# Optimization experiments

Hardware: AMD Instinct MI355X
Metric: run time of the kernel (lower is better)

The kernel has to match this reference:

```python
import jax, jax.numpy as jnp
import numpy as np

B, T, D_IN, D_OUT = 4, 2048, 1024, 1024


def setup_inputs() -> dict:
    key = jax.random.key(0)
    k1, k2, k3, k4 = jax.random.split(key, 4)
    s = 0.02  # keep activations in a sane range
    x = jax.random.normal(k1, (B, T, D_IN), dtype=jnp.float32)
    Wq = jax.random.normal(k2, (D_IN, D_OUT), dtype=jnp.float32) * s
    Wk = jax.random.normal(k3, (D_IN, D_OUT), dtype=jnp.float32) * s
    Wv = jax.random.normal(k4, (D_IN, D_OUT), dtype=jnp.float32) * s
    return {"x": x, "Wq": Wq, "Wk": Wk, "Wv": Wv}


def reference(x, Wq, Wk, Wv):
    # Linear projections (torch Linear: y = x @ W^T, here W stored as [d_in, d_out])
    q = jnp.einsum('btd,de->bte', x, Wq)
    k = jnp.einsum('btd,de,->bte', x, Wk, jnp.float32(1.0)) if False else jnp.einsum('btd,de->bte', x, Wk)
    v = jnp.einsum('btd,de->bte', x, Wv)
    # Full [B, T, T] score matrix (faithful to the hand-rolled implementation)
    scores = jnp.einsum('bqe,bke->bqk', q, k)
    T_ = x.shape[1]
    causal = jnp.triu(jnp.ones((T_, T_), dtype=bool), k=1)  # True above diagonal
    scores = jnp.where(causal[None, :, :], -jnp.inf, scores)
    scale = 1.0 / jnp.sqrt(jnp.asarray(k.shape[-1], dtype=scores.dtype))
    attn = jax.nn.softmax(scores * scale, axis=-1)
    # dropout p=0.0 -> identity
    return jnp.einsum('bqk,bke->bqe', attn, v)
```

## Files before the change

### kernel.cpp

```cpp
#include <hip/hip_runtime.h>
#include <hip/hip_bf16.h>
#include <cstdint>

typedef __attribute__((ext_vector_type(8))) short short8;
typedef __attribute__((ext_vector_type(4))) float floatx4;
typedef unsigned short ushort;

__device__ __forceinline__ float bf2f(ushort u) {
  unsigned int x = ((unsigned int)u) << 16;
  return __builtin_bit_cast(float, x);
}
__device__ __forceinline__ ushort f2bf(float f) {
  unsigned int x = __builtin_bit_cast(unsigned int, f);
  x += 0x7fffu + ((x >> 16) & 1u);
  return (ushort)(x >> 16);
}

__device__ __forceinline__ void gload_lds16(const void* g, void* l) {
  __builtin_amdgcn_global_load_lds(
      (const __attribute__((address_space(1))) void*)g,
      (__attribute__((address_space(3))) void*)l, 16, 0, 0);
}


__global__ __launch_bounds__(256) void cvtx_kernel(const float* __restrict__ x,
                                                   ushort* __restrict__ xb) {
  int i = blockIdx.x * 256 + threadIdx.x;
  const float4* xf = (const float4*)x;
  float4 a = xf[i * 2], b = xf[i * 2 + 1];
  short8 o;
  o[0] = (short)f2bf(a.x); o[1] = (short)f2bf(a.y);
  o[2] = (short)f2bf(a.z); o[3] = (short)f2bf(a.w);
  o[4] = (short)f2bf(b.x); o[5] = (short)f2bf(b.y);
  o[6] = (short)f2bf(b.z); o[7] = (short)f2bf(b.w);
  ((short8*)xb)[i] = o;
}

__global__ __launch_bounds__(256) void wt_kernel(const float* __restrict__ Wq,
                                                 const float* __restrict__ Wk,
                                                 const float* __restrict__ Wv,
                                                 ushort* __restrict__ Wt) {
  int z = blockIdx.z;
  const float* W = z == 0 ? Wq : (z == 1 ? Wk : Wv);
  ushort* O = Wt + (size_t)z * 1024 * 1024;
  __shared__ float tile[64][65];
  int c0 = blockIdx.x * 64;
  int r0 = blockIdx.y * 64;
  int tid = threadIdx.x;
#pragma unroll
  for (int i = 0; i < 4; ++i) {
    int c = tid + i * 256; int rr = c >> 4, q = c & 15;
    float4 v = *(const float4*)&W[(size_t)(r0 + rr) * 1024 + c0 + q * 4];
    tile[rr][q * 4 + 0] = v.x; tile[rr][q * 4 + 1] = v.y;
    tile[rr][q * 4 + 2] = v.z; tile[rr][q * 4 + 3] = v.w;
  }
  __syncthreads();
#pragma unroll
  for (int i = 0; i < 2; ++i) {
    int c = tid + i * 256; int oc = c >> 3, q = c & 7;
    short8 o;
#pragma unroll
    for (int j = 0; j < 8; ++j) o[j] = (short)f2bf(tile[q * 8 + j][oc]);
    *(short8*)&O[(size_t)(c0 + oc) * 1024 + r0 + q * 8] = o;
  }
}

__global__ __launch_bounds__(256) void vt_kernel(const ushort* __restrict__ V,
                                                 ushort* __restrict__ Vt) {
  int b = blockIdx.z;
  const ushort* Vb = V + (size_t)b * 2048 * 1024;
  ushort* Vtb = Vt + (size_t)b * 1024 * 2048;
  __shared__ ushort tile[64][72];
  int t0 = blockIdx.x * 64;
  int e0 = blockIdx.y * 64;
  int tid = threadIdx.x;
#pragma unroll
  for (int i = 0; i < 2; ++i) {
    int c = tid + i * 256; int rr = c >> 3, q = c & 7;
    short8 s = *(const short8*)&Vb[(size_t)(t0 + rr) * 1024 + e0 + q * 8];
#pragma unroll
    for (int j = 0; j < 8; ++j) tile[rr][q * 8 + j] = (ushort)s[j];
  }
  __syncthreads();
#pragma unroll
  for (int i = 0; i < 2; ++i) {
    int c = tid + i * 256; int er = c >> 3, q = c & 7;
    short8 o;
#pragma unroll
    for (int j = 0; j < 8; ++j) o[j] = (short)tile[q * 8 + j][er];
    *(short8*)&Vtb[(size_t)(e0 + er) * 2048 + t0 + q * 8] = o;
  }
}


__global__ __launch_bounds__(512, 2) void qkv8_kernel(const ushort* __restrict__ A,
                                                      const ushort* __restrict__ Bm,
                                                      ushort* __restrict__ QKV) {
  __shared__ __align__(16) ushort lds[2][2][2][8192];

  const int tid = threadIdx.x;
  const int lane = tid & 63;
  const int wave = tid >> 6;
  const int wm = wave >> 2;
  const int wn = wave & 3;
  const int r15 = lane & 15;
  const int kg = lane >> 4;

  const int nwgx = 32, nwgy = 12;
  int orig = blockIdx.y * nwgx + blockIdx.x;
  int swz = (orig & 7) * ((nwgx * nwgy) >> 3) + (orig >> 3);
  int by = swz % nwgy;
  int bx = swz / nwgy;
  const int m0 = bx * 256;
  const int n0 = by * 256;

  const ushort* Ag = A + (size_t)m0 * 1024;
  const ushort* Bg = Bm + (size_t)n0 * 1024;

  const int NKT = 16;

  floatx4 acc[8][4] = {};

  auto stage = [&](int sidx) {
    int kt = sidx >> 2, hh = sidx & 3;
    int mat = hh & 1, kh = hh >> 1;
    ushort* dst = &lds[kt & 1][mat][kh][0];
    const ushort* src = mat ? Bg : Ag;
    int kbase = kt * 64 + kh * 32;
#pragma unroll
    for (int i = 0; i < 2; ++i) {
      int t = tid + i * 512;
      int d = t * 16;
      int L = d ^ (((d >> 7) & 3) << 4);
      int row = L >> 6;
      int colE = (L & 63) >> 1;
      gload_lds16(src + (size_t)row * 1024 + kbase + colE, dst + t * 8);
    }
  };

  auto ldA = [&](int buf, int ks, int m) -> short8 {
    int row = wm * 128 + m * 16 + r15;
    int L = row * 64 + kg * 16;
    int P = L ^ (((row >> 1) & 3) << 4);
    return *(const short8*)((const char*)&lds[buf][0][ks][0] + P);
  };
  auto ldB = [&](int buf, int ks, int n) -> short8 {
    int row = wn * 64 + n * 16 + r15;
    int L = row * 64 + kg * 16;
    int P = L ^ (((row >> 1) & 3) << 4);
    return *(const short8*)((const char*)&lds[buf][1][ks][0] + P);
  };

  for (int s = 0; s < 6; ++s) stage(s);
  asm volatile("s_waitcnt vmcnt(8)" ::: "memory");
  __builtin_amdgcn_s_barrier();

  short8 bfrag[4];
  int sidx = 6;
  for (int kt = 0; kt < NKT; ++kt) {
    int cur = kt & 1;
#pragma unroll
    for (int q = 0; q < 4; ++q) {
      const int ks = q >> 1;
      const int msub = (q & 1) * 4;
      short8 afrag[4];
      if ((q & 1) == 0) {
#pragma unroll
        for (int n = 0; n < 4; ++n) bfrag[n] = ldB(cur, ks, n);
      }
#pragma unroll
      for (int m = 0; m < 4; ++m) afrag[m] = ldA(cur, ks, msub + m);
      if (sidx < NKT * 4) stage(sidx);
      ++sidx;
      if (q & 1) asm volatile("s_waitcnt vmcnt(4)" ::: "memory");
      __builtin_amdgcn_s_barrier();
      asm volatile("s_waitcnt lgkmcnt(0)" ::: "memory");
      __builtin_amdgcn_sched_barrier(0);
      __builtin_amdgcn_s_setprio(1);
#pragma unroll
      for (int m = 0; m < 4; ++m)
#pragma unroll
        for (int n = 0; n < 4; ++n)
          acc[msub + m][n] =
              __builtin_amdgcn_mfma_f32_16x16x32_bf16(afrag[m], bfrag[n], acc[msub + m][n], 0, 0, 0);
      __builtin_amdgcn_s_setprio(0);
      __builtin_amdgcn_s_barrier();
    }
  }

  ushort* Cz = QKV + (size_t)(n0 >> 10) * 8192 * 1024;
  const int cb = n0 & 1023;
  const int rq = kg * 4;
#pragma unroll
  for (int m = 0; m < 8; ++m) {
#pragma unroll
    for (int n = 0; n < 4; ++n) {
      int gc = cb + wn * 64 + n * 16 + r15;
#pragma unroll
      for (int r = 0; r < 4; ++r) {
        int gr = m0 + wm * 128 + m * 16 + rq + r;
        Cz[(size_t)gr * 1024 + gc] = f2bf(acc[m][n][r]);
      }
    }
  }
}


template <bool OUT_BF16>
__device__ __forceinline__ void gemm_tn_core(const ushort* __restrict__ A,
                                             const ushort* __restrict__ B,
                                             void* __restrict__ C,
                                             int lda, int ldb, int ldc,
                                             int m0, int n0, int kTiles) {
  __shared__ __align__(16) ushort Asm[2][128 * 32];
  __shared__ __align__(16) ushort Bsm[2][128 * 32];
  const int tid = threadIdx.x;
  const int lane = tid & 63;
  const int wave = tid >> 6;
  const int wrow = (wave >> 1) * 64;
  const int wcol = (wave & 1) * 64;
  const int r15 = lane & 15;
  const int kg = (lane >> 4) * 8;

  floatx4 acc[4][4] = {};

  const ushort* Ag = A + (size_t)m0 * lda;
  const ushort* Bg = B + (size_t)n0 * ldb;

  auto stage = [&](int buf, int kt) {
    int k0 = kt * 32;
#pragma unroll
    for (int i = 0; i < 2; ++i) {
      int c = tid + i * 256;
      gload_lds16(Ag + (size_t)(c >> 2) * lda + k0 + (c & 3) * 8, &Asm[buf][c * 8]);
    }
#pragma unroll
    for (int i = 0; i < 2; ++i) {
      int c = tid + i * 256;
      gload_lds16(Bg + (size_t)(c >> 2) * ldb + k0 + (c & 3) * 8, &Bsm[buf][c * 8]);
    }
  };

  stage(0, 0);
  for (int kt = 0; kt < kTiles; ++kt) {
    int cur = kt & 1;
    __syncthreads();
    if (kt + 1 < kTiles) stage(cur ^ 1, kt + 1);
    const ushort* As = Asm[cur];
    const ushort* Bs = Bsm[cur];
    short8 af[4], bfr[4];
#pragma unroll
    for (int m = 0; m < 4; ++m)
      af[m] = *(const short8*)&As[(wrow + m * 16 + r15) * 32 + kg];
#pragma unroll
    for (int n = 0; n < 4; ++n)
      bfr[n] = *(const short8*)&Bs[(wcol + n * 16 + r15) * 32 + kg];
#pragma unroll
    for (int m = 0; m < 4; ++m)
#pragma unroll
      for (int n = 0; n < 4; ++n)
        acc[m][n] = __builtin_amdgcn_mfma_f32_16x16x32_bf16(af[m], bfr[n], acc[m][n], 0, 0, 0);
  }

  const int rq = (lane >> 4) * 4;
#pragma unroll
  for (int m = 0; m < 4; ++m) {
#pragma unroll
    for (int n = 0; n < 4; ++n) {
      int gc = n0 + wcol + n * 16 + r15;
#pragma unroll
      for (int r = 0; r < 4; ++r) {
        int gr = m0 + wrow + m * 16 + rq + r;
        if (OUT_BF16)
          ((ushort*)C)[(size_t)gr * ldc + gc] = f2bf(acc[m][n][r]);
        else
          ((float*)C)[(size_t)gr * ldc + gc] = acc[m][n][r];
      }
    }
  }
}

__global__ __launch_bounds__(256) void s_kernel(const ushort* __restrict__ Q,
                                                const ushort* __restrict__ K,
                                                ushort* __restrict__ S) {
  int t = blockIdx.x;
  int qb = (int)((sqrtf(8.f * (float)t + 1.f) - 1.f) * 0.5f);
  while ((qb + 1) * (qb + 2) / 2 <= t) ++qb;
  while (qb * (qb + 1) / 2 > t) --qb;
  int kb = t - qb * (qb + 1) / 2;
  size_t b = blockIdx.y;
  gemm_tn_core<true>(Q + b * 2048 * 1024, K + b * 2048 * 1024, S + b * 2048 * 2048,
                     1024, 1024, 2048, qb * 128, kb * 128, 32);
}

__global__ __launch_bounds__(256) void pv_kernel(const ushort* __restrict__ P,
                                                 const ushort* __restrict__ Vt,
                                                 float* __restrict__ O) {
  int qb = blockIdx.x;
  size_t b = blockIdx.z;
  gemm_tn_core<false>(P + b * 2048 * 2048, Vt + b * 1024 * 2048, O + b * 2048 * 1024,
                      2048, 2048, 1024, qb * 128, blockIdx.y * 128, (qb + 1) * 4);
}

__global__ __launch_bounds__(256) void softmax_kernel(ushort* __restrict__ S) {
  const int r = blockIdx.x;
  const int b = blockIdx.y;
  ushort* row = S + ((size_t)b * 2048 + r) * 2048;
  const int len = r + 1;
  const int padEnd = ((r >> 7) + 1) << 7;
  const int tid = threadIdx.x;
  const int base = tid * 8;
  const float scale = 0.03125f;

  float v[8];
  float mymax = -1e30f;
  if (base < len) {
    short8 s = *(const short8*)(row + base);
#pragma unroll
    for (int j = 0; j < 8; ++j) {
      float f = (base + j < len) ? bf2f((ushort)s[j]) : -1e30f;
      v[j] = f;
      mymax = fmaxf(mymax, f);
    }
  } else {
#pragma unroll
    for (int j = 0; j < 8; ++j) v[j] = -1e30f;
  }

  __shared__ float redm[4], reds[4];
  const int wave = tid >> 6, lane = tid & 63;
#pragma unroll
  for (int off = 32; off > 0; off >>= 1) mymax = fmaxf(mymax, __shfl_xor(mymax, off, 64));
  if (lane == 0) redm[wave] = mymax;
  __syncthreads();
  float m = fmaxf(fmaxf(redm[0], redm[1]), fmaxf(redm[2], redm[3])) * scale;

  float p[8];
  float mysum = 0.f;
#pragma unroll
  for (int j = 0; j < 8; ++j) {
    float e = (base + j < len) ? __expf(v[j] * scale - m) : 0.f;
    p[j] = e;
    mysum += e;
  }
#pragma unroll
  for (int off = 32; off > 0; off >>= 1) mysum += __shfl_xor(mysum, off, 64);
  if (lane == 0) reds[wave] = mysum;
  __syncthreads();
  float inv = 1.f / (reds[0] + reds[1] + reds[2] + reds[3]);

  if (base < padEnd) {
    short8 o;
#pragma unroll
    for (int j = 0; j < 8; ++j) o[j] = (short)f2bf(p[j] * inv);
    *(short8*)(row + base) = o;
  }
}


extern "C" void kernel_launch(void* const* d_in, const int* in_sizes, int n_in,
                              void* d_out, int out_size, void* d_ws, size_t ws_size,
                              hipStream_t stream) {
  const float* x  = (const float*)d_in[0];
  const float* Wq = (const float*)d_in[1];
  const float* Wk = (const float*)d_in[2];
  const float* Wv = (const float*)d_in[3];
  float* out = (float*)d_out;

  ushort* Xb  = (ushort*)d_ws;
  ushort* Wt  = Xb + (size_t)8192 * 1024;
  ushort* QKV = Wt + (size_t)3 * 1024 * 1024;
  ushort* Vt  = QKV + (size_t)3 * 8192 * 1024;
  ushort* S   = Vt + (size_t)4 * 1024 * 2048;

  const ushort* Qp = QKV;
  const ushort* Kp = QKV + (size_t)8192 * 1024;
  const ushort* Vp = QKV + (size_t)2 * 8192 * 1024;

  hipLaunchKernelGGL(cvtx_kernel, dim3(4096), dim3(256), 0, stream, x, Xb);
  hipLaunchKernelGGL(wt_kernel, dim3(16, 16, 3), dim3(256), 0, stream, Wq, Wk, Wv, Wt);
  hipLaunchKernelGGL(qkv8_kernel, dim3(32, 12), dim3(512), 0, stream, Xb, Wt, QKV);
  hipLaunchKernelGGL(vt_kernel, dim3(32, 16, 4), dim3(256), 0, stream, Vp, Vt);
  hipLaunchKernelGGL(s_kernel, dim3(136, 4), dim3(256), 0, stream, Qp, Kp, S);
  hipLaunchKernelGGL(softmax_kernel, dim3(2048, 4), dim3(256), 0, stream, S);
  hipLaunchKernelGGL(pv_kernel, dim3(16, 8, 4), dim3(256), 0, stream, S, Vt, out);
}
```

Baseline: 188.7 us.

## Fuse V transpose into QKV GEMM epilogue and retile to 128x256 triple-buffered

```diff
diff --git a/kernel.cpp b/kernel.cpp
--- a/kernel.cpp
+++ b/kernel.cpp
@@ -3,6 +3,7 @@
 #include <cstdint>
 
 typedef __attribute__((ext_vector_type(8))) short short8;
+typedef __attribute__((ext_vector_type(4))) short short4v;
 typedef __attribute__((ext_vector_type(4))) float floatx4;
 typedef unsigned short ushort;
 
@@ -65,141 +66,147 @@
   }
 }
 
-__global__ __launch_bounds__(256) void vt_kernel(const ushort* __restrict__ V,
-                                                 ushort* __restrict__ Vt) {
-  int b = blockIdx.z;
-  const ushort* Vb = V + (size_t)b * 2048 * 1024;
-  ushort* Vtb = Vt + (size_t)b * 1024 * 2048;
-  __shared__ ushort tile[64][72];
-  int t0 = blockIdx.x * 64;
-  int e0 = blockIdx.y * 64;
-  int tid = threadIdx.x;
-#pragma unroll
-  for (int i = 0; i < 2; ++i) {
-    int c = tid + i * 256; int rr = c >> 3, q = c & 7;
-    short8 s = *(const short8*)&Vb[(size_t)(t0 + rr) * 1024 + e0 + q * 8];
-#pragma unroll
-    for (int j = 0; j < 8; ++j) tile[rr][q * 8 + j] = (ushort)s[j];
-  }
-  __syncthreads();
-#pragma unroll
-  for (int i = 0; i < 2; ++i) {
-    int c = tid + i * 256; int er = c >> 3, q = c & 7;
-    short8 o;
-#pragma unroll
-    for (int j = 0; j < 8; ++j) o[j] = (short)tile[q * 8 + j][er];
-    *(short8*)&Vtb[(size_t)(e0 + er) * 2048 + t0 + q * 8] = o;
-  }
-}
-
-
-__global__ __launch_bounds__(512, 2) void qkv8_kernel(const ushort* __restrict__ A,
+
+__global__ __launch_bounds__(256, 2) void qkv2_kernel(const ushort* __restrict__ A,
                                                       const ushort* __restrict__ Bm,
-                                                      ushort* __restrict__ QKV) {
-  __shared__ __align__(16) ushort lds[2][2][2][8192];
+                                                      ushort* __restrict__ Qo,
+                                                      ushort* __restrict__ Ko,
+                                                      ushort* __restrict__ Vt) {
+  __shared__ __align__(16) ushort ldsA[3][128 * 32];
+  __shared__ __align__(16) ushort ldsB[3][256 * 32];
 
   const int tid = threadIdx.x;
   const int lane = tid & 63;
   const int wave = tid >> 6;
-  const int wm = wave >> 2;
-  const int wn = wave & 3;
   const int r15 = lane & 15;
   const int kg = lane >> 4;
 
-  const int nwgx = 32, nwgy = 12;
-  int orig = blockIdx.y * nwgx + blockIdx.x;
-  int swz = (orig & 7) * ((nwgx * nwgy) >> 3) + (orig >> 3);
-  int by = swz % nwgy;
-  int bx = swz / nwgy;
-  const int m0 = bx * 256;
+  int orig = blockIdx.y * 64 + blockIdx.x;
+  int swz = (orig & 7) * 96 + (orig >> 3);
+  int bx = swz / 12;
+  int by = swz % 12;
+  const int m0 = bx * 128;
   const int n0 = by * 256;
 
   const ushort* Ag = A + (size_t)m0 * 1024;
   const ushort* Bg = Bm + (size_t)n0 * 1024;
 
-  const int NKT = 16;
+  const int NKT = 32;
 
   floatx4 acc[8][4] = {};
 
-  auto stage = [&](int sidx) {
-    int kt = sidx >> 2, hh = sidx & 3;
-    int mat = hh & 1, kh = hh >> 1;
-    ushort* dst = &lds[kt & 1][mat][kh][0];
-    const ushort* src = mat ? Bg : Ag;
-    int kbase = kt * 64 + kh * 32;
+  auto stage = [&](int kt, int slot) {
+    int k0 = kt * 32;
 #pragma unroll
     for (int i = 0; i < 2; ++i) {
-      int t = tid + i * 512;
-      int d = t * 16;
+      int c = tid + i * 256;
+      int d = c * 16;
       int L = d ^ (((d >> 7) & 3) << 4);
-      int row = L >> 6;
-      int colE = (L & 63) >> 1;
-      gload_lds16(src + (size_t)row * 1024 + kbase + colE, dst + t * 8);
+      gload_lds16(Ag + (size_t)(L >> 6) * 1024 + k0 + ((L & 63) >> 1),
+                  &ldsA[slot][c * 8]);
+    }
+#pragma unroll
+    for (int i = 0; i < 4; ++i) {
+      int c = tid + i * 256;
+      int d = c * 16;
+      int L = d ^ (((d >> 7) & 3) << 4);
+      gload_lds16(Bg + (size_t)(L >> 6) * 1024 + k0 + ((L & 63) >> 1),
+                  &ldsB[slot][c * 8]);
     }
   };
 
-  auto ldA = [&](int buf, int ks, int m) -> short8 {
-    int row = wm * 128 + m * 16 + r15;
-    int L = row * 64 + kg * 16;
-    int P = L ^ (((row >> 1) & 3) << 4);
-    return *(const short8*)((const char*)&lds[buf][0][ks][0] + P);
+  auto ldA = [&](int slot, int m) -> short8 {
+    int row = m * 16 + r15;
+    int P = (row * 64 + kg * 16) ^ (((row >> 1) & 3) << 4);
+    return *(const short8*)((const char*)&ldsA[slot][0] + P);
   };
-  auto ldB = [&](int buf, int ks, int n) -> short8 {
-    int row = wn * 64 + n * 16 + r15;
-    int L = row * 64 + kg * 16;
-    int P = L ^ (((row >> 1) & 3) << 4);
-    return *(const short8*)((const char*)&lds[buf][1][ks][0] + P);
+  auto ldB = [&](int slot, int n) -> short8 {
+    int row = wave * 64 + n * 16 + r15;
+    int P = (row * 64 + kg * 16) ^ (((row >> 1) & 3) << 4);
+    return *(const short8*)((const char*)&ldsB[slot][0] + P);
   };
 
-  for (int s = 0; s < 6; ++s) stage(s);
-  asm volatile("s_waitcnt vmcnt(8)" ::: "memory");
+  stage(0, 0);
+  stage(1, 1);
+  asm volatile("s_waitcnt vmcnt(6)" ::: "memory");
   __builtin_amdgcn_s_barrier();
 
-  short8 bfrag[4];
-  int sidx = 6;
+  int cur = 0;
   for (int kt = 0; kt < NKT; ++kt) {
-    int cur = kt & 1;
-#pragma unroll
-    for (int q = 0; q < 4; ++q) {
-      const int ks = q >> 1;
-      const int msub = (q & 1) * 4;
-      short8 afrag[4];
-      if ((q & 1) == 0) {
-#pragma unroll
-        for (int n = 0; n < 4; ++n) bfrag[n] = ldB(cur, ks, n);
+    short8 bfrag[4], afrag[4];
+#pragma unroll
+    for (int n = 0; n < 4; ++n) bfrag[n] = ldB(cur, n);
+#pragma unroll
+    for (int m = 0; m < 4; ++m) afrag[m] = ldA(cur, m);
+    if (kt + 2 < NKT) {
+      int slot = cur + 2; if (slot >= 3) slot -= 3;
+      stage(kt + 2, slot);
+    }
+    __builtin_amdgcn_s_barrier();
+    asm volatile("s_waitcnt lgkmcnt(0)" ::: "memory");
+    __builtin_amdgcn_sched_barrier(0);
+    __builtin_amdgcn_s_setprio(1);
+#pragma unroll
+    for (int m = 0; m < 4; ++m)
+#pragma unroll
+      for (int n = 0; n < 4; ++n)
+        acc[m][n] = __builtin_amdgcn_mfma_f32_16x16x32_bf16(afrag[m], bfrag[n], acc[m][n], 0, 0, 0);
+    __builtin_amdgcn_s_setprio(0);
+    __builtin_amdgcn_s_barrier();
+
+#pragma unroll
+    for (int m = 0; m < 4; ++m) afrag[m] = ldA(cur, m + 4);
+    if (kt >= NKT - 3) {
+      asm volatile("s_waitcnt vmcnt(0)" ::: "memory");
+    } else {
+      asm volatile("s_waitcnt vmcnt(6)" ::: "memory");
+    }
+    __builtin_amdgcn_s_barrier();
+    asm volatile("s_waitcnt lgkmcnt(0)" ::: "memory");
+    __builtin_amdgcn_sched_barrier(0);
+    __builtin_amdgcn_s_setprio(1);
+#pragma unroll
+    for (int m = 0; m < 4; ++m)
+#pragma unroll
+      for (int n = 0; n < 4; ++n)
+        acc[m + 4][n] = __builtin_amdgcn_mfma_f32_16x16x32_bf16(afrag[m], bfrag[n], acc[m + 4][n], 0, 0, 0);
+    __builtin_amdgcn_s_setprio(0);
+    __builtin_amdgcn_s_barrier();
+
+    ++cur; if (cur >= 3) cur = 0;
+  }
+
+  const int z = n0 >> 10;
+  const int rq = kg * 4;
+  if (z < 2) {
+    ushort* Cz = z == 0 ? Qo : Ko;
+    const int cb = n0 & 1023;
+#pragma unroll
+    for (int m = 0; m < 8; ++m) {
+#pragma unroll
+      for (int n = 0; n < 4; ++n) {
+        int gc = cb + wave * 64 + n * 16 + r15;
+#pragma unroll
+        for (int r = 0; r < 4; ++r) {
+          int gr = m0 + m * 16 + rq + r;
+          Cz[(size_t)gr * 1024 + gc] = f2bf(acc[m][n][r]);
+        }
       }
-#pragma unroll
-      for (int m = 0; m < 4; ++m) afrag[m] = ldA(cur, ks, msub + m);
-      if (sidx < NKT * 4) stage(sidx);
-      ++sidx;
-      if (q & 1) asm volatile("s_waitcnt vmcnt(4)" ::: "memory");
-      __builtin_amdgcn_s_barrier();
-      asm volatile("s_waitcnt lgkmcnt(0)" ::: "memory");
-      __builtin_amdgcn_sched_barrier(0);
-      __builtin_amdgcn_s_setprio(1);
-#pragma unroll
-      for (int m = 0; m < 4; ++m)
-#pragma unroll
-        for (int n = 0; n < 4; ++n)
-          acc[msub + m][n] =
-              __builtin_amdgcn_mfma_f32_16x16x32_bf16(afrag[m], bfrag[n], acc[msub + m][n], 0, 0, 0);
-      __builtin_amdgcn_s_setprio(0);
-      __builtin_amdgcn_s_barrier();
-    }
-  }
-
-  ushort* Cz = QKV + (size_t)(n0 >> 10) * 8192 * 1024;
-  const int cb = n0 & 1023;
-  const int rq = kg * 4;
-#pragma unroll
-  for (int m = 0; m < 8; ++m) {
-#pragma unroll
-    for (int n = 0; n < 4; ++n) {
-      int gc = cb + wn * 64 + n * 16 + r15;
-#pragma unroll
-      for (int r = 0; r < 4; ++r) {
-        int gr = m0 + wm * 128 + m * 16 + rq + r;
-        Cz[(size_t)gr * 1024 + gc] = f2bf(acc[m][n][r]);
+    }
+  } else {
+#pragma unroll
+    for (int m = 0; m < 8; ++m) {
+      int gr = m0 + m * 16 + rq;
+      int b = gr >> 11;
+      int t = gr & 2047;
+      ushort* Vb = Vt + (size_t)b * 1024 * 2048;
+#pragma unroll
+      for (int n = 0; n < 4; ++n) {
+        int e = (n0 - 2048) + wave * 64 + n * 16 + r15;
+        short4v o;
+#pragma unroll
+        for (int r = 0; r < 4; ++r) o[r] = (short)f2bf(acc[m][n][r]);
+        *(short4v*)&Vb[(size_t)e * 2048 + t] = o;
       }
     }
   }
@@ -369,18 +376,16 @@
 
   ushort* Xb  = (ushort*)d_ws;
   ushort* Wt  = Xb + (size_t)8192 * 1024;
-  ushort* QKV = Wt + (size_t)3 * 1024 * 1024;
-  ushort* Vt  = QKV + (size_t)3 * 8192 * 1024;
+  ushort* QK  = Wt + (size_t)3 * 1024 * 1024;
+  ushort* Vt  = QK + (size_t)2 * 8192 * 1024;
   ushort* S   = Vt + (size_t)4 * 1024 * 2048;
 
-  const ushort* Qp = QKV;
-  const ushort* Kp = QKV + (size_t)8192 * 1024;
-  const ushort* Vp = QKV + (size_t)2 * 8192 * 1024;
+  ushort* Qp = QK;
+  ushort* Kp = QK + (size_t)8192 * 1024;
 
   hipLaunchKernelGGL(cvtx_kernel, dim3(4096), dim3(256), 0, stream, x, Xb);
   hipLaunchKernelGGL(wt_kernel, dim3(16, 16, 3), dim3(256), 0, stream, Wq, Wk, Wv, Wt);
-  hipLaunchKernelGGL(qkv8_kernel, dim3(32, 12), dim3(512), 0, stream, Xb, Wt, QKV);
-  hipLaunchKernelGGL(vt_kernel, dim3(32, 16, 4), dim3(256), 0, stream, Vp, Vt);
+  hipLaunchKernelGGL(qkv2_kernel, dim3(64, 12), dim3(256), 0, stream, Xb, Wt, Qp, Kp, Vt);
   hipLaunchKernelGGL(s_kernel, dim3(136, 4), dim3(256), 0, stream, Qp, Kp, S);
   hipLaunchKernelGGL(softmax_kernel, dim3(2048, 4), dim3(256), 0, stream, S);
   hipLaunchKernelGGL(pv_kernel, dim3(16, 8, 4), dim3(256), 0, stream, S, Vt, out);
```

Result: no change. 187.3 us (-0.7%).

## Fuse prep kernels, write V transposed from QKV GEMM, reverse PV block order

Applied to the files above, without the earlier changes.

```diff
diff --git a/kernel.cpp b/kernel.cpp
--- a/kernel.cpp
+++ b/kernel.cpp
@@ -3,6 +3,7 @@
 #include <cstdint>
 
 typedef __attribute__((ext_vector_type(8))) short short8;
+typedef __attribute__((ext_vector_type(4))) short short4v;
 typedef __attribute__((ext_vector_type(4))) float floatx4;
 typedef unsigned short ushort;
 
@@ -23,79 +24,58 @@
 }
 
 
-__global__ __launch_bounds__(256) void cvtx_kernel(const float* __restrict__ x,
-                                                   ushort* __restrict__ xb) {
-  int i = blockIdx.x * 256 + threadIdx.x;
-  const float4* xf = (const float4*)x;
-  float4 a = xf[i * 2], b = xf[i * 2 + 1];
-  short8 o;
-  o[0] = (short)f2bf(a.x); o[1] = (short)f2bf(a.y);
-  o[2] = (short)f2bf(a.z); o[3] = (short)f2bf(a.w);
-  o[4] = (short)f2bf(b.x); o[5] = (short)f2bf(b.y);
-  o[6] = (short)f2bf(b.z); o[7] = (short)f2bf(b.w);
-  ((short8*)xb)[i] = o;
-}
-
-__global__ __launch_bounds__(256) void wt_kernel(const float* __restrict__ Wq,
-                                                 const float* __restrict__ Wk,
-                                                 const float* __restrict__ Wv,
-                                                 ushort* __restrict__ Wt) {
-  int z = blockIdx.z;
-  const float* W = z == 0 ? Wq : (z == 1 ? Wk : Wv);
-  ushort* O = Wt + (size_t)z * 1024 * 1024;
-  __shared__ float tile[64][65];
-  int c0 = blockIdx.x * 64;
-  int r0 = blockIdx.y * 64;
+__global__ __launch_bounds__(256) void prep_kernel(const float* __restrict__ x,
+                                                   const float* __restrict__ Wq,
+                                                   const float* __restrict__ Wk,
+                                                   const float* __restrict__ Wv,
+                                                   ushort* __restrict__ xb,
+                                                   ushort* __restrict__ Wt) {
+  int bid = blockIdx.x;
   int tid = threadIdx.x;
-#pragma unroll
-  for (int i = 0; i < 4; ++i) {
-    int c = tid + i * 256; int rr = c >> 4, q = c & 15;
-    float4 v = *(const float4*)&W[(size_t)(r0 + rr) * 1024 + c0 + q * 4];
-    tile[rr][q * 4 + 0] = v.x; tile[rr][q * 4 + 1] = v.y;
-    tile[rr][q * 4 + 2] = v.z; tile[rr][q * 4 + 3] = v.w;
-  }
-  __syncthreads();
-#pragma unroll
-  for (int i = 0; i < 2; ++i) {
-    int c = tid + i * 256; int oc = c >> 3, q = c & 7;
+  if (bid < 4096) {
+    int i = bid * 256 + tid;
+    const float4* xf = (const float4*)x;
+    float4 a = xf[i * 2], b = xf[i * 2 + 1];
     short8 o;
-#pragma unroll
-    for (int j = 0; j < 8; ++j) o[j] = (short)f2bf(tile[q * 8 + j][oc]);
-    *(short8*)&O[(size_t)(c0 + oc) * 1024 + r0 + q * 8] = o;
-  }
-}
-
-__global__ __launch_bounds__(256) void vt_kernel(const ushort* __restrict__ V,
-                                                 ushort* __restrict__ Vt) {
-  int b = blockIdx.z;
-  const ushort* Vb = V + (size_t)b * 2048 * 1024;
-  ushort* Vtb = Vt + (size_t)b * 1024 * 2048;
-  __shared__ ushort tile[64][72];
-  int t0 = blockIdx.x * 64;
-  int e0 = blockIdx.y * 64;
-  int tid = threadIdx.x;
-#pragma unroll
-  for (int i = 0; i < 2; ++i) {
-    int c = tid + i * 256; int rr = c >> 3, q = c & 7;
-    short8 s = *(const short8*)&Vb[(size_t)(t0 + rr) * 1024 + e0 + q * 8];
-#pragma unroll
-    for (int j = 0; j < 8; ++j) tile[rr][q * 8 + j] = (ushort)s[j];
-  }
-  __syncthreads();
-#pragma unroll
-  for (int i = 0; i < 2; ++i) {
-    int c = tid + i * 256; int er = c >> 3, q = c & 7;
-    short8 o;
-#pragma unroll
-    for (int j = 0; j < 8; ++j) o[j] = (short)tile[q * 8 + j][er];
-    *(short8*)&Vtb[(size_t)(e0 + er) * 2048 + t0 + q * 8] = o;
+    o[0] = (short)f2bf(a.x); o[1] = (short)f2bf(a.y);
+    o[2] = (short)f2bf(a.z); o[3] = (short)f2bf(a.w);
+    o[4] = (short)f2bf(b.x); o[5] = (short)f2bf(b.y);
+    o[6] = (short)f2bf(b.z); o[7] = (short)f2bf(b.w);
+    ((short8*)xb)[i] = o;
+  } else {
+    int t = bid - 4096;
+    int z = t >> 8;
+    int rem = t & 255;
+    int c0 = (rem & 15) * 64;
+    int r0 = (rem >> 4) * 64;
+    const float* W = z == 0 ? Wq : (z == 1 ? Wk : Wv);
+    ushort* O = Wt + (size_t)z * 1024 * 1024;
+    __shared__ float tile[64][65];
+#pragma unroll
+    for (int i = 0; i < 4; ++i) {
+      int c = tid + i * 256; int rr = c >> 4, q = c & 15;
+      float4 v = *(const float4*)&W[(size_t)(r0 + rr) * 1024 + c0 + q * 4];
+      tile[rr][q * 4 + 0] = v.x; tile[rr][q * 4 + 1] = v.y;
+      tile[rr][q * 4 + 2] = v.z; tile[rr][q * 4 + 3] = v.w;
+    }
+    __syncthreads();
+#pragma unroll
+    for (int i = 0; i < 2; ++i) {
+      int c = tid + i * 256; int oc = c >> 3, q = c & 7;
+      short8 o;
+#pragma unroll
+      for (int j = 0; j < 8; ++j) o[j] = (short)f2bf(tile[q * 8 + j][oc]);
+      *(short8*)&O[(size_t)(c0 + oc) * 1024 + r0 + q * 8] = o;
+    }
   }
 }
 
 
 __global__ __launch_bounds__(512, 2) void qkv8_kernel(const ushort* __restrict__ A,
                                                       const ushort* __restrict__ Bm,
-                                                      ushort* __restrict__ QKV) {
+                                                      ushort* __restrict__ Qo,
+                                                      ushort* __restrict__ Ko,
+                                                      ushort* __restrict__ Vt) {
   __shared__ __align__(16) ushort lds[2][2][2][8192];
 
   const int tid = threadIdx.x;
@@ -188,18 +168,37 @@
     }
   }
 
-  ushort* Cz = QKV + (size_t)(n0 >> 10) * 8192 * 1024;
-  const int cb = n0 & 1023;
+  const int z = n0 >> 10;
   const int rq = kg * 4;
-#pragma unroll
-  for (int m = 0; m < 8; ++m) {
-#pragma unroll
-    for (int n = 0; n < 4; ++n) {
-      int gc = cb + wn * 64 + n * 16 + r15;
-#pragma unroll
-      for (int r = 0; r < 4; ++r) {
-        int gr = m0 + wm * 128 + m * 16 + rq + r;
-        Cz[(size_t)gr * 1024 + gc] = f2bf(acc[m][n][r]);
+  if (z < 2) {
+    ushort* Cz = z == 0 ? Qo : Ko;
+    const int cb = n0 & 1023;
+#pragma unroll
+    for (int m = 0; m < 8; ++m) {
+#pragma unroll
+      for (int n = 0; n < 4; ++n) {
+        int gc = cb + wn * 64 + n * 16 + r15;
+#pragma unroll
+        for (int r = 0; r < 4; ++r) {
+          int gr = m0 + wm * 128 + m * 16 + rq + r;
+          Cz[(size_t)gr * 1024 + gc] = f2bf(acc[m][n][r]);
+        }
+      }
+    }
+  } else {
+#pragma unroll
+    for (int m = 0; m < 8; ++m) {
+      int gr = m0 + wm * 128 + m * 16 + rq;
+      int b = gr >> 11;
+      int t = gr & 2047;
+      ushort* Vb = Vt + (size_t)b * 1024 * 2048;
+#pragma unroll
+      for (int n = 0; n < 4; ++n) {
+        int e = (n0 - 2048) + wn * 64 + n * 16 + r15;
+        short4v o;
+#pragma unroll
+        for (int r = 0; r < 4; ++r) o[r] = (short)f2bf(acc[m][n][r]);
+        *(short4v*)&Vb[(size_t)e * 2048 + t] = o;
       }
     }
   }
@@ -296,7 +295,7 @@
 __global__ __launch_bounds__(256) void pv_kernel(const ushort* __restrict__ P,
                                                  const ushort* __restrict__ Vt,
                                                  float* __restrict__ O) {
-  int qb = blockIdx.x;
+  int qb = 15 - blockIdx.x;
   size_t b = blockIdx.z;
   gemm_tn_core<false>(P + b * 2048 * 2048, Vt + b * 1024 * 2048, O + b * 2048 * 1024,
                       2048, 2048, 1024, qb * 128, blockIdx.y * 128, (qb + 1) * 4);
@@ -369,18 +368,15 @@
 
   ushort* Xb  = (ushort*)d_ws;
   ushort* Wt  = Xb + (size_t)8192 * 1024;
-  ushort* QKV = Wt + (size_t)3 * 1024 * 1024;
-  ushort* Vt  = QKV + (size_t)3 * 8192 * 1024;
+  ushort* QK  = Wt + (size_t)3 * 1024 * 1024;
+  ushort* Vt  = QK + (size_t)2 * 8192 * 1024;
   ushort* S   = Vt + (size_t)4 * 1024 * 2048;
 
-  const ushort* Qp = QKV;
-  const ushort* Kp = QKV + (size_t)8192 * 1024;
-  const ushort* Vp = QKV + (size_t)2 * 8192 * 1024;
-
-  hipLaunchKernelGGL(cvtx_kernel, dim3(4096), dim3(256), 0, stream, x, Xb);
-  hipLaunchKernelGGL(wt_kernel, dim3(16, 16, 3), dim3(256), 0, stream, Wq, Wk, Wv, Wt);
-  hipLaunchKernelGGL(qkv8_kernel, dim3(32, 12), dim3(512), 0, stream, Xb, Wt, QKV);
-  hipLaunchKernelGGL(vt_kernel, dim3(32, 16, 4), dim3(256), 0, stream, Vp, Vt);
+  ushort* Qp = QK;
+  ushort* Kp = QK + (size_t)8192 * 1024;
+
+  hipLaunchKernelGGL(prep_kernel, dim3(4864), dim3(256), 0, stream, x, Wq, Wk, Wv, Xb, Wt);
+  hipLaunchKernelGGL(qkv8_kernel, dim3(32, 12), dim3(512), 0, stream, Xb, Wt, Qp, Kp, Vt);
   hipLaunchKernelGGL(s_kernel, dim3(136, 4), dim3(256), 0, stream, Qp, Kp, S);
   hipLaunchKernelGGL(softmax_kernel, dim3(2048, 4), dim3(256), 0, stream, S);
   hipLaunchKernelGGL(pv_kernel, dim3(16, 8, 4), dim3(256), 0, stream, S, Vt, out);
```

Measured after the change: 184.5 us. 1.02x faster.
